# Optimization experiments

Hardware: AMD Instinct MI355X
Metric: run time of the kernel (lower is better)

## Reference

```python
import jax, jax.numpy as jnp
import numpy as np

N_CELLS = 500_000
B = 512
D_X = 128
D_Z = 32
D_IN = D_X + D_Z  # 160
H = 256
D_OUT = 16


def _linear_params(key, fan_in, fan_out):
    k1, k2 = jax.random.split(key)
    bound = 1.0 / np.sqrt(fan_in)
    W = jax.random.uniform(k1, (fan_in, fan_out), jnp.float32, -bound, bound)
    b = jax.random.uniform(k2, (fan_out,), jnp.float32, -bound, bound)
    return W, b


def setup_inputs() -> dict:
    key = jax.random.key(0)
    ks = jax.random.split(key, 8)
    X = jax.random.uniform(ks[0], (N_CELLS, D_X), jnp.float32)  # nonneg counts-like
    Z = jax.random.normal(ks[1], (B, D_Z), jnp.float32)
    cell_to_batch = jax.random.randint(ks[2], (N_CELLS,), 0, B, jnp.int64)
    sample_idx_batch = jnp.arange(B, dtype=jnp.int64)
    W1, b1 = _linear_params(ks[3], D_IN, H)
    W2, b2 = _linear_params(ks[4], H, H)
    W3, b3 = _linear_params(ks[5], H, D_OUT)
    return {"X": X, "Z": Z, "W1": W1, "b1": b1, "W2": W2, "b2": b2,
            "W3": W3, "b3": b3, "cell_to_batch": cell_to_batch,
            "sample_idx_batch": sample_idx_batch}


def reference(X, Z, W1, b1, W2, b2, W3, b3, cell_to_batch, sample_idx_batch):
    # gather per-sample covariates to per-cell rows
    Zc = Z[cell_to_batch]                              # [N, D_Z]
    seg = sample_idx_batch[cell_to_batch]              # [N] remapped sample ids
    # preprocessor: log-normalize X, concat covariates
    Xp = jnp.concatenate([jnp.log1p(X), Zc], axis=-1)  # [N, D_IN]
    # cell predictor MLP (Linear-ReLU x2 + Linear)
    h = jax.nn.relu(Xp @ W1 + b1)
    h = jax.nn.relu(h @ W2 + b2)
    X_cell = h @ W3 + b3                               # [N, D_OUT]
    # aggregator: segment mean over cells of each sample
    nseg = sample_idx_batch.shape[0]
    sums = jax.ops.segment_sum(X_cell, seg, num_segments=nseg)
    counts = jax.ops.segment_sum(jnp.ones((X_cell.shape[0], 1), X_cell.dtype), seg, num_segments=nseg)
    Y_sample = sums / jnp.maximum(counts, 1.0)
    # postprocessor: identity
    return Y_sample
```

## Files before the change

kernel.cpp:

```cpp
#include <hip/hip_runtime.h>
#include <hip/hip_bf16.h>

typedef __attribute__((ext_vector_type(8))) short short8;
typedef __attribute__((ext_vector_type(4))) float floatx4;

#define N_CELLS  500000
#define B_SAMP   512
#define D_X      128
#define D_Z      32
#define D_IN     160
#define H_DIM    256
#define D_OUT    16

#define M_TILE   32
#define LDA      168
#define LDH      264

#define NREP     64

#define OFF_W1P   0
#define OFF_W2P   81920
#define OFF_W3P   212992
#define OFF_ACC   221184
#define OFF_CNT   2318336

__global__ void pack_w(const float* __restrict__ W, __hip_bfloat16* __restrict__ dst,
                       int N, int kS) {
    int idx = blockIdx.x * blockDim.x + threadIdx.x;
    int j = idx & 7;
    int L = (idx >> 3) & 63;
    int s = (idx >> 9) % kS;
    int t = idx / (kS << 9);
    int k = s * 32 + ((L >> 4) << 3) + j;
    int n = t * 16 + (L & 15);
    dst[idx] = __float2bfloat16(W[(size_t)k * N + n]);
}

__global__ void zero_ws(float* __restrict__ p, int n) {
    int i = blockIdx.x * blockDim.x + threadIdx.x;
    if (i < n) p[i] = 0.0f;
}

__global__ __launch_bounds__(256, 3)
void fused_mlp(const float* __restrict__ X, const float* __restrict__ Z,
               const int* __restrict__ c2b, const int* __restrict__ sidx,
               const float* __restrict__ b1, const float* __restrict__ b2,
               const float* __restrict__ b3,
               const __hip_bfloat16* __restrict__ w1p,
               const __hip_bfloat16* __restrict__ w2p,
               const __hip_bfloat16* __restrict__ w3p,
               float* __restrict__ accs, float* __restrict__ cnts) {
    __shared__ __hip_bfloat16 sXp[M_TILE][LDA];
    __shared__ __hip_bfloat16 sH[2][M_TILE][LDH];
    __shared__ float sP[4][M_TILE][D_OUT];

    const int tid = threadIdx.x;
    const int w   = tid >> 6;
    const int L   = tid & 63;
    const int q   = L >> 4;
    const int ln  = L & 15;
    const int base = blockIdx.x * M_TILE;

#pragma unroll
    for (int i = 0; i < 4; ++i) {
        int idx = tid + i * 256;
        int row = idx >> 5;
        int c4  = idx & 31;
        float4 v = *(const float4*)(X + (size_t)(base + row) * D_X + c4 * 4);
        __hip_bfloat16* d = &sXp[row][c4 * 4];
        d[0] = __float2bfloat16(__logf(1.0f + v.x));
        d[1] = __float2bfloat16(__logf(1.0f + v.y));
        d[2] = __float2bfloat16(__logf(1.0f + v.z));
        d[3] = __float2bfloat16(__logf(1.0f + v.w));
    }
    {
        int row = tid >> 3;
        int c0  = (tid & 7) * 4;
        int b   = c2b[base + row];
        float4 v = *(const float4*)(Z + (size_t)b * D_Z + c0);
        __hip_bfloat16* d = &sXp[row][D_X + c0];
        d[0] = __float2bfloat16(v.x);
        d[1] = __float2bfloat16(v.y);
        d[2] = __float2bfloat16(v.z);
        d[3] = __float2bfloat16(v.w);
    }
    __syncthreads();

    floatx4 acc[2][4];
#pragma unroll
    for (int mt = 0; mt < 2; ++mt)
#pragma unroll
        for (int nt = 0; nt < 4; ++nt)
            acc[mt][nt] = (floatx4){0.f, 0.f, 0.f, 0.f};

    float bias1[4];
#pragma unroll
    for (int nt = 0; nt < 4; ++nt) bias1[nt] = b1[w * 64 + nt * 16 + ln];

#pragma unroll
    for (int s = 0; s < 5; ++s) {
        short8 a0 = *(const short8*)&sXp[ln][s * 32 + q * 8];
        short8 a1 = *(const short8*)&sXp[16 + ln][s * 32 + q * 8];
#pragma unroll
        for (int nt = 0; nt < 4; ++nt) {
            int t = w * 4 + nt;
            short8 bf = *(const short8*)(w1p + (size_t)(((t * 5 + s) << 6) + L) * 8);
            acc[0][nt] = __builtin_amdgcn_mfma_f32_16x16x32_bf16(a0, bf, acc[0][nt], 0, 0, 0);
            acc[1][nt] = __builtin_amdgcn_mfma_f32_16x16x32_bf16(a1, bf, acc[1][nt], 0, 0, 0);
        }
    }
#pragma unroll
    for (int mt = 0; mt < 2; ++mt)
#pragma unroll
        for (int nt = 0; nt < 4; ++nt)
#pragma unroll
            for (int r = 0; r < 4; ++r) {
                float v = fmaxf(acc[mt][nt][r] + bias1[nt], 0.0f);
                sH[0][mt * 16 + q * 4 + r][w * 64 + nt * 16 + ln] = __float2bfloat16(v);
            }
    __syncthreads();

#pragma unroll
    for (int mt = 0; mt < 2; ++mt)
#pragma unroll
        for (int nt = 0; nt < 4; ++nt)
            acc[mt][nt] = (floatx4){0.f, 0.f, 0.f, 0.f};

    float bias2[4];
#pragma unroll
    for (int nt = 0; nt < 4; ++nt) bias2[nt] = b2[w * 64 + nt * 16 + ln];

#pragma unroll
    for (int s = 0; s < 8; ++s) {
        short8 a0 = *(const short8*)&sH[0][ln][s * 32 + q * 8];
        short8 a1 = *(const short8*)&sH[0][16 + ln][s * 32 + q * 8];
#pragma unroll
        for (int nt = 0; nt < 4; ++nt) {
            int t = w * 4 + nt;
            short8 bf = *(const short8*)(w2p + (size_t)(((t * 8 + s) << 6) + L) * 8);
            acc[0][nt] = __builtin_amdgcn_mfma_f32_16x16x32_bf16(a0, bf, acc[0][nt], 0, 0, 0);
            acc[1][nt] = __builtin_amdgcn_mfma_f32_16x16x32_bf16(a1, bf, acc[1][nt], 0, 0, 0);
        }
    }
#pragma unroll
    for (int mt = 0; mt < 2; ++mt)
#pragma unroll
        for (int nt = 0; nt < 4; ++nt)
#pragma unroll
            for (int r = 0; r < 4; ++r) {
                float v = fmaxf(acc[mt][nt][r] + bias2[nt], 0.0f);
                sH[1][mt * 16 + q * 4 + r][w * 64 + nt * 16 + ln] = __float2bfloat16(v);
            }
    __syncthreads();

    floatx4 acc3[2];
    acc3[0] = (floatx4){0.f, 0.f, 0.f, 0.f};
    acc3[1] = (floatx4){0.f, 0.f, 0.f, 0.f};
#pragma unroll
    for (int ss = 0; ss < 2; ++ss) {
        int s = w * 2 + ss;
        short8 a0 = *(const short8*)&sH[1][ln][s * 32 + q * 8];
        short8 a1 = *(const short8*)&sH[1][16 + ln][s * 32 + q * 8];
        short8 bf = *(const short8*)(w3p + (size_t)((s << 6) + L) * 8);
        acc3[0] = __builtin_amdgcn_mfma_f32_16x16x32_bf16(a0, bf, acc3[0], 0, 0, 0);
        acc3[1] = __builtin_amdgcn_mfma_f32_16x16x32_bf16(a1, bf, acc3[1], 0, 0, 0);
    }
#pragma unroll
    for (int mt = 0; mt < 2; ++mt)
#pragma unroll
        for (int r = 0; r < 4; ++r)
            sP[w][mt * 16 + q * 4 + r][ln] = acc3[mt][r];
    __syncthreads();

    float* accR = accs + (size_t)(blockIdx.x & (NREP - 1)) * (B_SAMP * D_OUT);
    float* cntR = cnts + (size_t)(blockIdx.x & (NREP - 1)) * B_SAMP;
#pragma unroll
    for (int i = 0; i < 2; ++i) {
        int idx = tid + i * 256;
        int m = idx >> 4, n = idx & 15;
        float v = sP[0][m][n] + sP[1][m][n] + sP[2][m][n] + sP[3][m][n] + b3[n];
        int b = c2b[base + m];
        int s = sidx[b];
        atomicAdd(&accR[(size_t)s * D_OUT + n], v);
        if (n == 0) atomicAdd(&cntR[s], 1.0f);
    }
}

__global__ __launch_bounds__(256)
void finalize(const float* __restrict__ accs, const float* __restrict__ cnts,
              float* __restrict__ out) {
    int o = blockIdx.x * blockDim.x + threadIdx.x;
    int s = o >> 4;
    float sum = 0.f, cnt = 0.f;
#pragma unroll 8
    for (int r = 0; r < NREP; ++r) {
        sum += accs[(size_t)r * (B_SAMP * D_OUT) + o];
        cnt += cnts[(size_t)r * B_SAMP + s];
    }
    out[o] = sum / fmaxf(cnt, 1.0f);
}

extern "C" void kernel_launch(void* const* d_in, const int* in_sizes, int n_in,
                              void* d_out, int out_size, void* d_ws, size_t ws_size,
                              hipStream_t stream) {
    const float* X   = (const float*)d_in[0];
    const float* Z   = (const float*)d_in[1];
    const float* W1  = (const float*)d_in[2];
    const float* b1  = (const float*)d_in[3];
    const float* W2  = (const float*)d_in[4];
    const float* b2  = (const float*)d_in[5];
    const float* W3  = (const float*)d_in[6];
    const float* b3  = (const float*)d_in[7];
    const int*   c2b = (const int*)d_in[8];
    const int*   sidx= (const int*)d_in[9];

    char* ws = (char*)d_ws;
    __hip_bfloat16* w1p = (__hip_bfloat16*)(ws + OFF_W1P);
    __hip_bfloat16* w2p = (__hip_bfloat16*)(ws + OFF_W2P);
    __hip_bfloat16* w3p = (__hip_bfloat16*)(ws + OFF_W3P);
    float* accs = (float*)(ws + OFF_ACC);
    float* cnts = (float*)(ws + OFF_CNT);
    float* out  = (float*)d_out;

    {
        int nz = NREP * (B_SAMP * D_OUT + B_SAMP);
        zero_ws<<<(nz + 255) / 256, 256, 0, stream>>>(accs, nz);
    }

    pack_w<<<160, 256, 0, stream>>>(W1, w1p, H_DIM, 5);
    pack_w<<<256, 256, 0, stream>>>(W2, w2p, H_DIM, 8);
    pack_w<<<16,  256, 0, stream>>>(W3, w3p, D_OUT, 8);

    fused_mlp<<<N_CELLS / M_TILE, 256, 0, stream>>>(X, Z, c2b, sidx, b1, b2, b3,
                                                    w1p, w2p, w3p, accs, cnts);
    finalize<<<32, 256, 0, stream>>>(accs, cnts, out);
}
```

Baseline: 510.6 us.

## Convert fused MLP to persistent kernel with register-resident weights and LDS segment accumulators

Replaces the one-block-per-tile MLP with a persistent kernel of 256 blocks of 512 threads. Each block keeps its slice of W1/W2/W3 in registers, prefetches the next tile's X/Z into registers while computing the current one, and accumulates segment sums and counts in LDS. Per-block partials are written once, and finalize reduces them and adds b3 after the mean. This removes the per-tile global weight reloads, the zeroing kernel and the global atomics. In exchange it uses heavy register pressure and only 256 blocks, which may underfill the GPU, and it relies on LDS atomics.

```diff
diff --git a/kernel.cpp b/kernel.cpp
--- a/kernel.cpp
+++ b/kernel.cpp
@@ -2,6 +2,7 @@
 #include <hip/hip_bf16.h>
 
 typedef __attribute__((ext_vector_type(8))) short short8;
+typedef __attribute__((ext_vector_type(4))) short sv4;
 typedef __attribute__((ext_vector_type(4))) float floatx4;
 
 #define N_CELLS  500000
@@ -13,16 +14,16 @@
 #define D_OUT    16
 
 #define M_TILE   32
+#define N_TILES  (N_CELLS / M_TILE)
+#define GRID     256
 #define LDA      168
 #define LDH      264
-
-#define NREP     64
 
 #define OFF_W1P   0
 #define OFF_W2P   81920
 #define OFF_W3P   212992
-#define OFF_ACC   221184
-#define OFF_CNT   2318336
+#define OFF_PART  221184
+#define PART_STRIDE 8704
 
 __global__ void pack_w(const float* __restrict__ W, __hip_bfloat16* __restrict__ dst,
                        int N, int kS) {
@@ -36,168 +37,195 @@
     dst[idx] = __float2bfloat16(W[(size_t)k * N + n]);
 }
 
-__global__ void zero_ws(float* __restrict__ p, int n) {
-    int i = blockIdx.x * blockDim.x + threadIdx.x;
-    if (i < n) p[i] = 0.0f;
-}
-
-__global__ __launch_bounds__(256, 3)
-void fused_mlp(const float* __restrict__ X, const float* __restrict__ Z,
-               const int* __restrict__ c2b, const int* __restrict__ sidx,
-               const float* __restrict__ b1, const float* __restrict__ b2,
-               const float* __restrict__ b3,
-               const __hip_bfloat16* __restrict__ w1p,
-               const __hip_bfloat16* __restrict__ w2p,
-               const __hip_bfloat16* __restrict__ w3p,
-               float* __restrict__ accs, float* __restrict__ cnts) {
+static __device__ __forceinline__ short f2bf(float f) {
+    __hip_bfloat16 h = __float2bfloat16(f);
+    return *(short*)&h;
+}
+
+__global__ __launch_bounds__(512, 2)
+void fused_persist(const float* __restrict__ X, const float* __restrict__ Z,
+                   const int* __restrict__ c2b, const int* __restrict__ sidx,
+                   const float* __restrict__ b1, const float* __restrict__ b2,
+                   const __hip_bfloat16* __restrict__ w1p,
+                   const __hip_bfloat16* __restrict__ w2p,
+                   const __hip_bfloat16* __restrict__ w3p,
+                   float* __restrict__ part) {
     __shared__ __hip_bfloat16 sXp[M_TILE][LDA];
     __shared__ __hip_bfloat16 sH[2][M_TILE][LDH];
-    __shared__ float sP[4][M_TILE][D_OUT];
+    __shared__ float lAcc[B_SAMP * D_OUT];
+    __shared__ float lCnt[B_SAMP];
+    __shared__ int   sSeg[M_TILE];
 
     const int tid = threadIdx.x;
     const int w   = tid >> 6;
     const int L   = tid & 63;
     const int q   = L >> 4;
     const int ln  = L & 15;
-    const int base = blockIdx.x * M_TILE;
-
-#pragma unroll
-    for (int i = 0; i < 4; ++i) {
-        int idx = tid + i * 256;
-        int row = idx >> 5;
-        int c4  = idx & 31;
-        float4 v = *(const float4*)(X + (size_t)(base + row) * D_X + c4 * 4);
-        __hip_bfloat16* d = &sXp[row][c4 * 4];
-        d[0] = __float2bfloat16(__logf(1.0f + v.x));
-        d[1] = __float2bfloat16(__logf(1.0f + v.y));
-        d[2] = __float2bfloat16(__logf(1.0f + v.z));
-        d[3] = __float2bfloat16(__logf(1.0f + v.w));
-    }
+
+    for (int i = tid; i < B_SAMP * D_OUT; i += 512) lAcc[i] = 0.f;
+    for (int i = tid; i < B_SAMP; i += 512) lCnt[i] = 0.f;
+
+    short8 W1A[2][5], W2A[2][8], W3A;
+#pragma unroll
+    for (int nt = 0; nt < 2; ++nt)
+#pragma unroll
+        for (int s = 0; s < 5; ++s)
+            W1A[nt][s] = *(const short8*)(w1p + (size_t)((((2 * w + nt) * 5 + s) << 6) + L) * 8);
+#pragma unroll
+    for (int nt = 0; nt < 2; ++nt)
+#pragma unroll
+        for (int s = 0; s < 8; ++s)
+            W2A[nt][s] = *(const short8*)(w2p + (size_t)((((2 * w + nt) * 8 + s) << 6) + L) * 8);
+    W3A = *(const short8*)(w3p + (size_t)((w << 6) + L) * 8);
+
+    float4 bias1[2], bias2[2];
+#pragma unroll
+    for (int nt = 0; nt < 2; ++nt) {
+        bias1[nt] = *(const float4*)&b1[w * 32 + nt * 16 + q * 4];
+        bias2[nt] = *(const float4*)&b2[w * 32 + nt * 16 + q * 4];
+    }
+    __syncthreads();
+
+    const int rowx = tid >> 4, colx = (tid & 15) * 8;
+    const int rowz = (tid >> 3) & 31, colz = (tid & 7) * 4;
+    float4 xv0, xv1, zv;
+    int cb = 0;
     {
-        int row = tid >> 3;
-        int c0  = (tid & 7) * 4;
-        int b   = c2b[base + row];
-        float4 v = *(const float4*)(Z + (size_t)b * D_Z + c0);
-        __hip_bfloat16* d = &sXp[row][D_X + c0];
-        d[0] = __float2bfloat16(v.x);
-        d[1] = __float2bfloat16(v.y);
-        d[2] = __float2bfloat16(v.z);
-        d[3] = __float2bfloat16(v.w);
-    }
-    __syncthreads();
-
-    floatx4 acc[2][4];
-#pragma unroll
-    for (int mt = 0; mt < 2; ++mt)
-#pragma unroll
-        for (int nt = 0; nt < 4; ++nt)
-            acc[mt][nt] = (floatx4){0.f, 0.f, 0.f, 0.f};
-
-    float bias1[4];
-#pragma unroll
-    for (int nt = 0; nt < 4; ++nt) bias1[nt] = b1[w * 64 + nt * 16 + ln];
-
-#pragma unroll
-    for (int s = 0; s < 5; ++s) {
-        short8 a0 = *(const short8*)&sXp[ln][s * 32 + q * 8];
-        short8 a1 = *(const short8*)&sXp[16 + ln][s * 32 + q * 8];
-#pragma unroll
-        for (int nt = 0; nt < 4; ++nt) {
-            int t = w * 4 + nt;
-            short8 bf = *(const short8*)(w1p + (size_t)(((t * 5 + s) << 6) + L) * 8);
-            acc[0][nt] = __builtin_amdgcn_mfma_f32_16x16x32_bf16(a0, bf, acc[0][nt], 0, 0, 0);
-            acc[1][nt] = __builtin_amdgcn_mfma_f32_16x16x32_bf16(a1, bf, acc[1][nt], 0, 0, 0);
-        }
-    }
-#pragma unroll
-    for (int mt = 0; mt < 2; ++mt)
-#pragma unroll
-        for (int nt = 0; nt < 4; ++nt)
-#pragma unroll
-            for (int r = 0; r < 4; ++r) {
-                float v = fmaxf(acc[mt][nt][r] + bias1[nt], 0.0f);
-                sH[0][mt * 16 + q * 4 + r][w * 64 + nt * 16 + ln] = __float2bfloat16(v);
-            }
-    __syncthreads();
-
-#pragma unroll
-    for (int mt = 0; mt < 2; ++mt)
-#pragma unroll
-        for (int nt = 0; nt < 4; ++nt)
-            acc[mt][nt] = (floatx4){0.f, 0.f, 0.f, 0.f};
-
-    float bias2[4];
-#pragma unroll
-    for (int nt = 0; nt < 4; ++nt) bias2[nt] = b2[w * 64 + nt * 16 + ln];
-
-#pragma unroll
-    for (int s = 0; s < 8; ++s) {
-        short8 a0 = *(const short8*)&sH[0][ln][s * 32 + q * 8];
-        short8 a1 = *(const short8*)&sH[0][16 + ln][s * 32 + q * 8];
-#pragma unroll
-        for (int nt = 0; nt < 4; ++nt) {
-            int t = w * 4 + nt;
-            short8 bf = *(const short8*)(w2p + (size_t)(((t * 8 + s) << 6) + L) * 8);
-            acc[0][nt] = __builtin_amdgcn_mfma_f32_16x16x32_bf16(a0, bf, acc[0][nt], 0, 0, 0);
-            acc[1][nt] = __builtin_amdgcn_mfma_f32_16x16x32_bf16(a1, bf, acc[1][nt], 0, 0, 0);
-        }
-    }
-#pragma unroll
-    for (int mt = 0; mt < 2; ++mt)
-#pragma unroll
-        for (int nt = 0; nt < 4; ++nt)
-#pragma unroll
-            for (int r = 0; r < 4; ++r) {
-                float v = fmaxf(acc[mt][nt][r] + bias2[nt], 0.0f);
-                sH[1][mt * 16 + q * 4 + r][w * 64 + nt * 16 + ln] = __float2bfloat16(v);
-            }
-    __syncthreads();
-
-    floatx4 acc3[2];
-    acc3[0] = (floatx4){0.f, 0.f, 0.f, 0.f};
-    acc3[1] = (floatx4){0.f, 0.f, 0.f, 0.f};
-#pragma unroll
-    for (int ss = 0; ss < 2; ++ss) {
-        int s = w * 2 + ss;
-        short8 a0 = *(const short8*)&sH[1][ln][s * 32 + q * 8];
-        short8 a1 = *(const short8*)&sH[1][16 + ln][s * 32 + q * 8];
-        short8 bf = *(const short8*)(w3p + (size_t)((s << 6) + L) * 8);
-        acc3[0] = __builtin_amdgcn_mfma_f32_16x16x32_bf16(a0, bf, acc3[0], 0, 0, 0);
-        acc3[1] = __builtin_amdgcn_mfma_f32_16x16x32_bf16(a1, bf, acc3[1], 0, 0, 0);
-    }
-#pragma unroll
-    for (int mt = 0; mt < 2; ++mt)
-#pragma unroll
-        for (int r = 0; r < 4; ++r)
-            sP[w][mt * 16 + q * 4 + r][ln] = acc3[mt][r];
-    __syncthreads();
-
-    float* accR = accs + (size_t)(blockIdx.x & (NREP - 1)) * (B_SAMP * D_OUT);
-    float* cntR = cnts + (size_t)(blockIdx.x & (NREP - 1)) * B_SAMP;
-#pragma unroll
-    for (int i = 0; i < 2; ++i) {
-        int idx = tid + i * 256;
-        int m = idx >> 4, n = idx & 15;
-        float v = sP[0][m][n] + sP[1][m][n] + sP[2][m][n] + sP[3][m][n] + b3[n];
-        int b = c2b[base + m];
-        int s = sidx[b];
-        atomicAdd(&accR[(size_t)s * D_OUT + n], v);
-        if (n == 0) atomicAdd(&cntR[s], 1.0f);
-    }
+        int base = blockIdx.x * M_TILE;
+        const float* xr = X + (size_t)(base + rowx) * D_X + colx;
+        xv0 = *(const float4*)xr;
+        xv1 = *(const float4*)(xr + 4);
+        cb  = c2b[base + rowz];
+        if (tid < 256) zv = *(const float4*)(Z + (size_t)cb * D_Z + colz);
+    }
+
+    for (int tt = blockIdx.x; tt < N_TILES; tt += GRID) {
+        {
+            short8 pk;
+            pk[0] = f2bf(__logf(1.0f + xv0.x)); pk[1] = f2bf(__logf(1.0f + xv0.y));
+            pk[2] = f2bf(__logf(1.0f + xv0.z)); pk[3] = f2bf(__logf(1.0f + xv0.w));
+            pk[4] = f2bf(__logf(1.0f + xv1.x)); pk[5] = f2bf(__logf(1.0f + xv1.y));
+            pk[6] = f2bf(__logf(1.0f + xv1.z)); pk[7] = f2bf(__logf(1.0f + xv1.w));
+            *(short8*)&sXp[rowx][colx] = pk;
+            if (tid < 256) {
+                sv4 zp;
+                zp[0] = f2bf(zv.x); zp[1] = f2bf(zv.y);
+                zp[2] = f2bf(zv.z); zp[3] = f2bf(zv.w);
+                *(sv4*)&sXp[rowz][D_X + colz] = zp;
+                if ((tid & 7) == 0) {
+                    int s = sidx[cb];
+                    sSeg[rowz] = s;
+                    atomicAdd(&lCnt[s], 1.0f);
+                }
+            }
+        }
+        __syncthreads();
+
+        {
+            int tn = tt + GRID;
+            if (tn < N_TILES) {
+                int nb = tn * M_TILE;
+                const float* xr = X + (size_t)(nb + rowx) * D_X + colx;
+                xv0 = *(const float4*)xr;
+                xv1 = *(const float4*)(xr + 4);
+                cb  = c2b[nb + rowz];
+                if (tid < 256) zv = *(const float4*)(Z + (size_t)cb * D_Z + colz);
+            }
+        }
+
+        floatx4 acc[2][2];
+#pragma unroll
+        for (int nt = 0; nt < 2; ++nt)
+#pragma unroll
+            for (int ct = 0; ct < 2; ++ct)
+                acc[nt][ct] = (floatx4){0.f, 0.f, 0.f, 0.f};
+#pragma unroll
+        for (int s = 0; s < 5; ++s) {
+            short8 x0 = *(const short8*)&sXp[ln][s * 32 + q * 8];
+            short8 x1 = *(const short8*)&sXp[16 + ln][s * 32 + q * 8];
+#pragma unroll
+            for (int nt = 0; nt < 2; ++nt) {
+                acc[nt][0] = __builtin_amdgcn_mfma_f32_16x16x32_bf16(W1A[nt][s], x0, acc[nt][0], 0, 0, 0);
+                acc[nt][1] = __builtin_amdgcn_mfma_f32_16x16x32_bf16(W1A[nt][s], x1, acc[nt][1], 0, 0, 0);
+            }
+        }
+#pragma unroll
+        for (int nt = 0; nt < 2; ++nt)
+#pragma unroll
+            for (int ct = 0; ct < 2; ++ct) {
+                sv4 pk;
+                pk[0] = f2bf(fmaxf(acc[nt][ct][0] + bias1[nt].x, 0.f));
+                pk[1] = f2bf(fmaxf(acc[nt][ct][1] + bias1[nt].y, 0.f));
+                pk[2] = f2bf(fmaxf(acc[nt][ct][2] + bias1[nt].z, 0.f));
+                pk[3] = f2bf(fmaxf(acc[nt][ct][3] + bias1[nt].w, 0.f));
+                *(sv4*)&sH[0][ct * 16 + ln][w * 32 + nt * 16 + q * 4] = pk;
+            }
+        __syncthreads();
+
+#pragma unroll
+        for (int nt = 0; nt < 2; ++nt)
+#pragma unroll
+            for (int ct = 0; ct < 2; ++ct)
+                acc[nt][ct] = (floatx4){0.f, 0.f, 0.f, 0.f};
+#pragma unroll
+        for (int s = 0; s < 8; ++s) {
+            short8 x0 = *(const short8*)&sH[0][ln][s * 32 + q * 8];
+            short8 x1 = *(const short8*)&sH[0][16 + ln][s * 32 + q * 8];
+#pragma unroll
+            for (int nt = 0; nt < 2; ++nt) {
+                acc[nt][0] = __builtin_amdgcn_mfma_f32_16x16x32_bf16(W2A[nt][s], x0, acc[nt][0], 0, 0, 0);
+                acc[nt][1] = __builtin_amdgcn_mfma_f32_16x16x32_bf16(W2A[nt][s], x1, acc[nt][1], 0, 0, 0);
+            }
+        }
+#pragma unroll
+        for (int nt = 0; nt < 2; ++nt)
+#pragma unroll
+            for (int ct = 0; ct < 2; ++ct) {
+                sv4 pk;
+                pk[0] = f2bf(fmaxf(acc[nt][ct][0] + bias2[nt].x, 0.f));
+                pk[1] = f2bf(fmaxf(acc[nt][ct][1] + bias2[nt].y, 0.f));
+                pk[2] = f2bf(fmaxf(acc[nt][ct][2] + bias2[nt].z, 0.f));
+                pk[3] = f2bf(fmaxf(acc[nt][ct][3] + bias2[nt].w, 0.f));
+                *(sv4*)&sH[1][ct * 16 + ln][w * 32 + nt * 16 + q * 4] = pk;
+            }
+        __syncthreads();
+
+        {
+            floatx4 a3[2];
+            a3[0] = (floatx4){0.f, 0.f, 0.f, 0.f};
+            a3[1] = (floatx4){0.f, 0.f, 0.f, 0.f};
+            short8 x0 = *(const short8*)&sH[1][ln][w * 32 + q * 8];
+            short8 x1 = *(const short8*)&sH[1][16 + ln][w * 32 + q * 8];
+            a3[0] = __builtin_amdgcn_mfma_f32_16x16x32_bf16(W3A, x0, a3[0], 0, 0, 0);
+            a3[1] = __builtin_amdgcn_mfma_f32_16x16x32_bf16(W3A, x1, a3[1], 0, 0, 0);
+#pragma unroll
+            for (int ct = 0; ct < 2; ++ct) {
+                int seg = sSeg[ct * 16 + ln];
+#pragma unroll
+                for (int r = 0; r < 4; ++r)
+                    atomicAdd(&lAcc[seg * D_OUT + q * 4 + r], a3[ct][r]);
+            }
+        }
+        __syncthreads();
+    }
+
+    float* dst = part + (size_t)blockIdx.x * PART_STRIDE;
+    for (int i = tid; i < B_SAMP * D_OUT; i += 512) dst[i] = lAcc[i];
+    if (tid < B_SAMP) dst[B_SAMP * D_OUT + tid] = lCnt[tid];
 }
 
 __global__ __launch_bounds__(256)
-void finalize(const float* __restrict__ accs, const float* __restrict__ cnts,
+void finalize(const float* __restrict__ part, const float* __restrict__ b3,
               float* __restrict__ out) {
     int o = blockIdx.x * blockDim.x + threadIdx.x;
     int s = o >> 4;
     float sum = 0.f, cnt = 0.f;
 #pragma unroll 8
-    for (int r = 0; r < NREP; ++r) {
-        sum += accs[(size_t)r * (B_SAMP * D_OUT) + o];
-        cnt += cnts[(size_t)r * B_SAMP + s];
-    }
-    out[o] = sum / fmaxf(cnt, 1.0f);
+    for (int c = 0; c < GRID; ++c) {
+        sum += part[(size_t)c * PART_STRIDE + o];
+        cnt += part[(size_t)c * PART_STRIDE + B_SAMP * D_OUT + s];
+    }
+    out[o] = (cnt > 0.f) ? (sum / cnt + b3[o & 15]) : 0.f;
 }
 
 extern "C" void kernel_launch(void* const* d_in, const int* in_sizes, int n_in,
@@ -218,20 +246,14 @@
     __hip_bfloat16* w1p = (__hip_bfloat16*)(ws + OFF_W1P);
     __hip_bfloat16* w2p = (__hip_bfloat16*)(ws + OFF_W2P);
     __hip_bfloat16* w3p = (__hip_bfloat16*)(ws + OFF_W3P);
-    float* accs = (float*)(ws + OFF_ACC);
-    float* cnts = (float*)(ws + OFF_CNT);
+    float* part = (float*)(ws + OFF_PART);
     float* out  = (float*)d_out;
-
-    {
-        int nz = NREP * (B_SAMP * D_OUT + B_SAMP);
-        zero_ws<<<(nz + 255) / 256, 256, 0, stream>>>(accs, nz);
-    }
 
     pack_w<<<160, 256, 0, stream>>>(W1, w1p, H_DIM, 5);
     pack_w<<<256, 256, 0, stream>>>(W2, w2p, H_DIM, 8);
     pack_w<<<16,  256, 0, stream>>>(W3, w3p, D_OUT, 8);
 
-    fused_mlp<<<N_CELLS / M_TILE, 256, 0, stream>>>(X, Z, c2b, sidx, b1, b2, b3,
-                                                    w1p, w2p, w3p, accs, cnts);
-    finalize<<<32, 256, 0, stream>>>(accs, cnts, out);
-}
+    fused_persist<<<GRID, 512, 0, stream>>>(X, Z, c2b, sidx, b1, b2,
+                                            w1p, w2p, w3p, part);
+    finalize<<<32, 256, 0, stream>>>(part, b3, out);
+}
```

Result: slower. 764.8 us (+49.8%).
